# Kernel optimization log

Measured on AMD Instinct MI355X. Metric: run time of the kernel, lower is better.

## Reference

```python
import jax, jax.numpy as jnp
import numpy as np

NPOINT = 2048
RADII = (0.4, 0.8)
NSAMPLES = (16, 32)
EPS = 1e-5


def _fps(xyz, npoint):
    # iterative farthest point sampling, start at index 0 (matches CUDA kernel)
    B, N, _ = xyz.shape

    def step(carry, _):
        dist, last = carry  # dist [B,N], last [B]
        lx = jnp.take_along_axis(xyz, last[:, None, None], axis=1)  # [B,1,3]
        d = jnp.sum((xyz - lx) ** 2, axis=-1)  # [B,N]
        dist = jnp.minimum(dist, d)
        nxt = jnp.argmax(dist, axis=1).astype(jnp.int32)
        return (dist, nxt), last

    init = (jnp.full((B, N), 1e10, xyz.dtype), jnp.zeros((B,), jnp.int32))
    _, idxs = jax.lax.scan(step, init, None, length=npoint)
    return idxs.T  # [B, npoint]


def _ball_query(radius, nsample, xyz, new_xyz):
    # first-nsample points within radius, in original order; pad with first hit (0 if none)
    N = xyz.shape[1]
    d2 = jnp.sum((new_xyz[:, :, None, :] - xyz[:, None, :, :]) ** 2, axis=-1)  # [B,S,N]
    mask = d2 < radius * radius
    ar = jnp.arange(N, dtype=jnp.int32)
    key = jnp.where(mask, ar, N + ar)  # in-range first, stable original order
    order = jnp.argsort(key, axis=-1)[..., :nsample].astype(jnp.int32)  # [B,S,ns]
    cnt = mask.sum(axis=-1, keepdims=True)  # [B,S,1]
    valid = jnp.arange(nsample) < cnt
    return jnp.where(valid, order, order[..., :1])


def _bn_relu(x):
    # training-mode BatchNorm (gamma=1, beta=0) over all dims but channel (last)
    red = tuple(range(x.ndim - 1))
    mu = x.mean(axis=red, keepdims=True)
    var = x.var(axis=red, keepdims=True)
    return jax.nn.relu((x - mu) * jax.lax.rsqrt(var + EPS))


def _scale(xyz, new_xyz, feats, radius, nsample, ws):
    idx = _ball_query(radius, nsample, xyz, new_xyz)  # [B,S,ns]
    B, S, ns = idx.shape
    flat = idx.reshape(B, S * ns)
    gx = jnp.take_along_axis(xyz, flat[..., None], axis=1).reshape(B, S, ns, 3)
    gx = gx - new_xyz[:, :, None, :]  # relative coords
    gf = jnp.take_along_axis(feats, flat[..., None], axis=1).reshape(B, S, ns, -1)
    h = jnp.concatenate([gx, gf], axis=-1)  # [B,S,ns,3+C]
    for w in ws:
        h = _bn_relu(h @ w)  # pointwise conv (kernel 1) + BN + ReLU
    return h.max(axis=2)  # max-pool over group -> [B,S,Cout]


def setup_inputs() -> dict:
    key = jax.random.key(0)
    ks = jax.random.split(key, 16)
    s = 0.02
    return {
        "xyz": jax.random.normal(ks[0], (8, 8192, 3), jnp.float32),
        "features": jax.random.normal(ks[1], (8, 8192, 64), jnp.float32),
        "w0_0": jax.random.normal(ks[2], (67, 64), jnp.float32) * s,
        "w0_1": jax.random.normal(ks[3], (64, 64), jnp.float32) * s,
        "w0_2": jax.random.normal(ks[4], (64, 128), jnp.float32) * s,
        "w1_0": jax.random.normal(ks[5], (67, 64), jnp.float32) * s,
        "w1_1": jax.random.normal(ks[6], (64, 64), jnp.float32) * s,
        "w1_2": jax.random.normal(ks[7], (64, 128), jnp.float32) * s,
        "agg_w": jax.random.normal(ks[8], (256, 256), jnp.float32) * s,
        "agg_b": jax.random.normal(ks[9], (256,), jnp.float32) * s,
        "conf_w": jax.random.normal(ks[10], (256, 256), jnp.float32) * s,
        "cls_w": jax.random.normal(ks[11], (256, 3), jnp.float32) * s,
        "cls_b": jax.random.normal(ks[12], (3,), jnp.float32) * s,
    }


def reference(xyz, features, w0_0, w0_1, w0_2, w1_0, w1_1, w1_2,
              agg_w, agg_b, conf_w, cls_w, cls_b):
    idx = _fps(xyz, NPOINT)  # [B,S]
    new_xyz = jnp.take_along_axis(xyz, idx[..., None], axis=1)  # [B,S,3]
    f0 = _scale(xyz, new_xyz, features, RADII[0], NSAMPLES[0], (w0_0, w0_1, w0_2))
    f1 = _scale(xyz, new_xyz, features, RADII[1], NSAMPLES[1], (w1_0, w1_1, w1_2))
    h = jnp.concatenate([f0, f1], axis=-1)  # [B,S,256]
    h = _bn_relu(h @ agg_w + agg_b)  # aggregation Linear + BN + ReLU
    c = _bn_relu(h @ conf_w)  # confidence hidden layer
    cls = c @ cls_w + cls_b  # [B,S,num_class]
    return new_xyz, h, cls
```

## Files before the change

### kernel.cpp

```cpp
#include <hip/hip_runtime.h>
#include <cstdint>
#include <cstddef>

constexpr int Bb = 8;
constexpr int Nn = 8192;
constexpr int Ss = 2048;
constexpr int BS = Bb * Ss;

typedef float vfloat2 __attribute__((ext_vector_type(2)));

__global__ __launch_bounds__(1024) void fps_kernel(const float* __restrict__ xyz,
                                                   float* __restrict__ new_xyz) {
  __shared__ float lx[Nn * 3];
  __shared__ int sidx[Ss];
  __shared__ unsigned long long slotV[2];
  __shared__ int slotI[2];
  const int b = blockIdx.x;
  const int tid = threadIdx.x;
  const float* xb = xyz + (size_t)b * Nn * 3;
  for (int e = tid; e < Nn * 3; e += 1024) lx[e] = xb[e];
  if (tid == 0) {
    slotV[0] = 0ull; slotV[1] = 0ull;
    slotI[0] = 0x7fffffff; slotI[1] = 0x7fffffff;
  }
  __syncthreads();

  vfloat2 px2[4], py2[4], pz2[4], df2[4];
  double dist[8];
#pragma unroll
  for (int jj = 0; jj < 4; ++jj) {
    const int p0 = tid + (2 * jj) * 1024, p1 = tid + (2 * jj + 1) * 1024;
    px2[jj] = (vfloat2){lx[p0 * 3 + 0], lx[p1 * 3 + 0]};
    py2[jj] = (vfloat2){lx[p0 * 3 + 1], lx[p1 * 3 + 1]};
    pz2[jj] = (vfloat2){lx[p0 * 3 + 2], lx[p1 * 3 + 2]};
    df2[jj] = (vfloat2){3.0e38f, 3.0e38f};
    dist[2 * jj] = 1e10;
    dist[2 * jj + 1] = 1e10;
  }
  float lmax = 3.0e38f;
  int cur = 0;
  double lv = -1.0;
  int li = 0x7fffffff;
  float lv32 = -1.0f;
  float wv32_c = -1.0f;
  for (int i = 0; i < Ss; ++i) {
    if (tid == 0) sidx[i] = cur;
    const float cxf = lx[cur * 3 + 0], cyf = lx[cur * 3 + 1], czf = lx[cur * 3 + 2];
    const vfloat2 cx2 = {cxf, cxf}, cy2 = {cyf, cyf}, cz2 = {czf, czf};
    vfloat2 d2v[4];
#pragma unroll
    for (int jj = 0; jj < 4; ++jj) {
      const vfloat2 dx = px2[jj] - cx2;
      const vfloat2 dy = py2[jj] - cy2;
      const vfloat2 dz = pz2[jj] - cz2;
      d2v[jj] = dx * dx + dy * dy + dz * dz;
    }
    const float dmin = fminf(fminf(fminf(d2v[0].x, d2v[0].y), fminf(d2v[1].x, d2v[1].y)),
                             fminf(fminf(d2v[2].x, d2v[2].y), fminf(d2v[3].x, d2v[3].y)));
    bool changed = false;
    if (dmin <= lmax) {
#pragma unroll
      for (int j = 0; j < 8; ++j) {
        const float d2s = d2v[j >> 1][j & 1];
        const float dfs = (j & 1) ? df2[j >> 1].y : df2[j >> 1].x;
        if (d2s <= dfs) {
          const float pxs = px2[j >> 1][j & 1];
          const float pys = py2[j >> 1][j & 1];
          const float pzs = pz2[j >> 1][j & 1];
          double dx = __dsub_rn((double)pxs, (double)cxf);
          double dy = __dsub_rn((double)pys, (double)cyf);
          double dz = __dsub_rn((double)pzs, (double)czf);
          double d = __dadd_rn(__dadd_rn(__dmul_rn(dx, dx), __dmul_rn(dy, dy)),
                               __dmul_rn(dz, dz));
          if (d < dist[j]) {
            dist[j] = d;
            const float dfn = (float)d * 1.000002f;
            if (j & 1) df2[j >> 1].y = dfn; else df2[j >> 1].x = dfn;
            changed = true;
          }
        }
      }
      if (changed) {
        lv = -1.0;
        li = 0;
#pragma unroll
        for (int j = 0; j < 8; ++j) {
          if (dist[j] > lv) { lv = dist[j]; li = tid + j * 1024; }
        }
        lv32 = (float)lv;
        lmax = fmaxf(fmaxf(fmaxf(df2[0].x, df2[0].y), fmaxf(df2[1].x, df2[1].y)),
                     fmaxf(fmaxf(df2[2].x, df2[2].y), fmaxf(df2[3].x, df2[3].y)));
      }
    }
    const unsigned long long anyb = __ballot(changed);
    if (anyb) {
      float m32 = lv32;
#pragma unroll
      for (int off = 1; off < 64; off <<= 1) m32 = fmaxf(m32, __shfl_xor(m32, off));
      wv32_c = m32;
    }
    const int pb = i & 1;
    if (lv32 == wv32_c) atomicMax(&slotV[pb], (unsigned long long)__double_as_longlong(lv));
    __syncthreads();
    const double W = __longlong_as_double((long long)slotV[pb]);
    if (lv == W) atomicMin(&slotI[pb], li);
    if (tid == 0) {
      slotV[pb ^ 1] = 0ull;
      slotI[pb ^ 1] = 0x7fffffff;
    }
    __syncthreads();
    cur = slotI[pb];
  }
  __syncthreads();
  float* nxb = new_xyz + (size_t)b * Ss * 3;
  for (int e = tid; e < Ss * 3; e += 1024) {
    const int i = e / 3, c = e - i * 3;
    nxb[e] = lx[sidx[i] * 3 + c];
  }
}

__global__ __launch_bounds__(256) void ballq_kernel(const float* __restrict__ xyz,
                                                    const float* __restrict__ nxyz,
                                                    int* __restrict__ idx0,
                                                    int* __restrict__ idx1) {
  const int wid = threadIdx.x >> 6, lane = threadIdx.x & 63;
  const int bs = blockIdx.x * 4 + wid;
  const int b = bs >> 11;
  const float* xb = xyz + (size_t)b * Nn * 3;
  const double cx = (double)nxyz[bs * 3 + 0];
  const double cy = (double)nxyz[bs * 3 + 1];
  const double cz = (double)nxyz[bs * 3 + 2];
  const double R0 = 0.4 * 0.4, R1 = 0.8 * 0.8;
  int cnt0 = 0, cnt1 = 0, first0 = 0, first1 = 0;
  const unsigned long long lmask = (1ull << lane) - 1ull;
  for (int base = 0; base < Nn; base += 64) {
    const int p = base + lane;
    double dx = __dsub_rn((double)xb[p * 3 + 0], cx);
    double dy = __dsub_rn((double)xb[p * 3 + 1], cy);
    double dz = __dsub_rn((double)xb[p * 3 + 2], cz);
    double d2 = __dadd_rn(__dadd_rn(__dmul_rn(dx, dx), __dmul_rn(dy, dy)), __dmul_rn(dz, dz));
    const bool in0 = d2 < R0, in1 = d2 < R1;
    unsigned long long m0 = __ballot(in0);
    unsigned long long m1 = __ballot(in1);
    if (cnt0 < 16 && m0) {
      if (cnt0 == 0) first0 = base + __builtin_ctzll(m0);
      int r = (int)__popcll(m0 & lmask);
      if (in0 && cnt0 + r < 16) idx0[bs * 16 + cnt0 + r] = p;
      cnt0 += (int)__popcll(m0);
    }
    if (cnt1 < 32 && m1) {
      if (cnt1 == 0) first1 = base + __builtin_ctzll(m1);
      int r = (int)__popcll(m1 & lmask);
      if (in1 && cnt1 + r < 32) idx1[bs * 32 + cnt1 + r] = p;
      cnt1 += (int)__popcll(m1);
    }
    if (cnt0 >= 16 && cnt1 >= 32) break;
  }
  const int f0 = cnt0 < 16 ? cnt0 : 16;
  for (int j = f0 + lane; j < 16; j += 64) idx0[bs * 16 + j] = first0;
  const int f1 = cnt1 < 32 ? cnt1 : 32;
  for (int j = f1 + lane; j < 32; j += 64) idx1[bs * 32 + j] = first1;
}

template <int COUT, int KTOT, int MODE, int NS, bool POOL, bool BIAS>
__global__ __launch_bounds__(256) void mlp_gemm(
    const float* __restrict__ xin, const float* __restrict__ xin2,
    const float* __restrict__ bnp, const float* __restrict__ bnp2,
    const float* __restrict__ w, const float* __restrict__ bias,
    const int* __restrict__ gidx, const float* __restrict__ xyz,
    const float* __restrict__ nxyz, const float* __restrict__ feats,
    float* __restrict__ hw, float* __restrict__ out, float* __restrict__ P) {
  constexpr int KC = (KTOT <= 68) ? KTOT : 32;
  constexpr int NCH = (KTOT + KC - 1) / KC;
  constexpr int TC = COUT / 16;
  constexpr int XPAD = KC + 1;
  constexpr int XSZ = 64 * XPAD;
  constexpr int EPI = (POOL ? 48 : 32) * COUT;
  constexpr int SM = (XSZ + KC * COUT > EPI) ? (XSZ + KC * COUT) : EPI;
  __shared__ float smem[SM];
  float* xS = smem;
  float* wS = smem + XSZ;

  const int tid = threadIdx.x;
  const int cg = tid & 15, rg = tid >> 4;
  const int row0 = blockIdx.x * 64;
  float acc[4][TC];
#pragma unroll
  for (int i = 0; i < 4; ++i)
#pragma unroll
    for (int t = 0; t < TC; ++t) acc[i][t] = 0.f;

  for (int ch = 0; ch < NCH; ++ch) {
    const int k0 = ch * KC;
    if (ch) __syncthreads();
    for (int e = tid; e < 64 * KC; e += 256) {
      const int r = e / KC, kk = e - r * KC;
      const int kg = k0 + kk;
      const int rowg = row0 + r;
      float v;
      if constexpr (MODE == 0) {
        const int bs = rowg / NS;
        const int p = gidx[rowg];
        const int bb = bs >> 11;
        if (kg < 3)
          v = xyz[(bb * Nn + p) * 3 + kg] - nxyz[bs * 3 + kg];
        else
          v = feats[((bb * Nn + p) << 6) + (kg - 3)];
      } else if constexpr (MODE == 1) {
        v = fmaxf((xin[(size_t)rowg * 64 + kg] - bnp[kg]) * bnp[64 + kg], 0.f);
      } else if constexpr (MODE == 2) {
        if (kg < 128)
          v = fmaxf((xin[(size_t)rowg * 128 + kg] - bnp[kg]) * bnp[128 + kg], 0.f);
        else {
          const int k2 = kg - 128;
          v = fmaxf((xin2[(size_t)rowg * 128 + k2] - bnp2[k2]) * bnp2[128 + k2], 0.f);
        }
      } else {
        v = fmaxf((xin[(size_t)rowg * 256 + kg] - bnp[kg]) * bnp[256 + kg], 0.f);
        hw[(size_t)rowg * 256 + kg] = v;
      }
      xS[r * XPAD + kk] = v;
    }
    for (int e = tid; e < KC * COUT; e += 256) {
      const int kk = e / COUT, c = e - kk * COUT;
      wS[kk * COUT + c] = w[(size_t)(k0 + kk) * COUT + c];
    }
    __syncthreads();
    for (int kk = 0; kk < KC; ++kk) {
      float xr[4];
#pragma unroll
      for (int i = 0; i < 4; ++i) xr[i] = xS[(rg * 4 + i) * XPAD + kk];
#pragma unroll
      for (int t = 0; t < TC; t += 4) {
        const float4 wv = *(const float4*)&wS[kk * COUT + cg * TC + t];
#pragma unroll
        for (int i = 0; i < 4; ++i) {
          acc[i][t + 0] = fmaf(xr[i], wv.x, acc[i][t + 0]);
          acc[i][t + 1] = fmaf(xr[i], wv.y, acc[i][t + 1]);
          acc[i][t + 2] = fmaf(xr[i], wv.z, acc[i][t + 2]);
          acc[i][t + 3] = fmaf(xr[i], wv.w, acc[i][t + 3]);
        }
      }
    }
  }
  __syncthreads();
  if constexpr (BIAS) {
#pragma unroll
    for (int t = 0; t < TC; ++t) {
      const float bv = bias[cg * TC + t];
#pragma unroll
      for (int i = 0; i < 4; ++i) acc[i][t] += bv;
    }
  }
  float* ssum = smem;
  float* ssq = smem + 16 * COUT;
  float* pbuf = smem + 32 * COUT;
  const int colb = cg * TC;
#pragma unroll
  for (int t = 0; t < TC; ++t) {
    float s = 0.f, q = 0.f, m = -3.4e38f;
#pragma unroll
    for (int i = 0; i < 4; ++i) {
      const float v = acc[i][t];
      s += v;
      q = fmaf(v, v, q);
      m = fmaxf(m, v);
    }
    ssum[rg * COUT + colb + t] = s;
    ssq[rg * COUT + colb + t] = q;
    if constexpr (POOL) pbuf[rg * COUT + colb + t] = m;
  }
  __syncthreads();
  const int gX = gridDim.x;
  for (int c = tid; c < COUT; c += 256) {
    float s = 0.f, q = 0.f;
#pragma unroll
    for (int rr = 0; rr < 16; ++rr) {
      s += ssum[rr * COUT + c];
      q += ssq[rr * COUT + c];
    }
    P[(size_t)c * gX + blockIdx.x] = s;
    P[(size_t)(COUT + c) * gX + blockIdx.x] = q;
  }
  if constexpr (POOL) {
    constexpr int G = 64 / NS, RPG = NS / 4;
    for (int o = tid; o < G * COUT; o += 256) {
      const int g = o / COUT, c = o - g * COUT;
      float m = pbuf[(g * RPG) * COUT + c];
#pragma unroll
      for (int qq = 1; qq < RPG; ++qq) m = fmaxf(m, pbuf[(g * RPG + qq) * COUT + c]);
      out[(size_t)(blockIdx.x * G + g) * COUT + c] = m;
    }
  } else {
#pragma unroll
    for (int i = 0; i < 4; ++i) {
      float* op = out + (size_t)(row0 + rg * 4 + i) * COUT + colb;
#pragma unroll
      for (int t = 0; t < TC; t += 4) {
        *(float4*)(op + t) = make_float4(acc[i][t], acc[i][t + 1], acc[i][t + 2], acc[i][t + 3]);
      }
    }
  }
}

__global__ __launch_bounds__(256) void bn_finalize(const float* __restrict__ P, int gX,
                                                   int M, int C, float* __restrict__ bnp) {
  __shared__ double sh[512];
  const int c = blockIdx.x;
  const int tid = threadIdx.x;
  const float* psum = P + (size_t)c * gX;
  const float* psq = P + (size_t)(C + c) * gX;
  double s = 0, q = 0;
  for (int i = tid; i < gX; i += 256) {
    s += (double)psum[i];
    q += (double)psq[i];
  }
  sh[tid] = s;
  sh[256 + tid] = q;
  __syncthreads();
  for (int off = 128; off; off >>= 1) {
    if (tid < off) {
      sh[tid] += sh[tid + off];
      sh[256 + tid] += sh[256 + tid + off];
    }
    __syncthreads();
  }
  if (tid == 0) {
    const double invM = 1.0 / (double)M;
    const double mu = sh[0] * invM;
    const double var = sh[256] * invM - mu * mu;
    bnp[c] = (float)mu;
    bnp[C + c] = (float)(1.0 / sqrt(var + 1e-5));
  }
}

__global__ __launch_bounds__(256) void cls_kernel(const float* __restrict__ craw,
                                                  const float* __restrict__ bnp,
                                                  const float* __restrict__ clsw,
                                                  const float* __restrict__ clsb,
                                                  float* __restrict__ outc) {
  const int wid = threadIdx.x >> 6, lane = threadIdx.x & 63;
  const int row = blockIdx.x * 4 + wid;
  const float* cr = craw + (size_t)row * 256;
  float a0 = 0.f, a1 = 0.f, a2 = 0.f;
#pragma unroll 4
  for (int k = lane; k < 256; k += 64) {
    float x = fmaxf((cr[k] - bnp[k]) * bnp[256 + k], 0.f);
    a0 = fmaf(x, clsw[k * 3 + 0], a0);
    a1 = fmaf(x, clsw[k * 3 + 1], a1);
    a2 = fmaf(x, clsw[k * 3 + 2], a2);
  }
#pragma unroll
  for (int off = 32; off; off >>= 1) {
    a0 += __shfl_down(a0, off);
    a1 += __shfl_down(a1, off);
    a2 += __shfl_down(a2, off);
  }
  if (lane == 0) {
    outc[row * 3 + 0] = a0 + clsb[0];
    outc[row * 3 + 1] = a1 + clsb[1];
    outc[row * 3 + 2] = a2 + clsb[2];
  }
}

extern "C" void kernel_launch(void* const* d_in, const int* in_sizes, int n_in,
                              void* d_out, int out_size, void* d_ws, size_t ws_size,
                              hipStream_t stream) {
  (void)in_sizes; (void)n_in; (void)out_size; (void)ws_size;
  const float* xyz = (const float*)d_in[0];
  const float* feats = (const float*)d_in[1];
  const float* w00 = (const float*)d_in[2];
  const float* w01 = (const float*)d_in[3];
  const float* w02 = (const float*)d_in[4];
  const float* w10 = (const float*)d_in[5];
  const float* w11 = (const float*)d_in[6];
  const float* w12 = (const float*)d_in[7];
  const float* aggw = (const float*)d_in[8];
  const float* aggb = (const float*)d_in[9];
  const float* confw = (const float*)d_in[10];
  const float* clsw = (const float*)d_in[11];
  const float* clsb = (const float*)d_in[12];

  float* outp = (float*)d_out;
  float* nxyz = outp;
  float* hout = outp + (size_t)BS * 3;
  float* clsout = hout + (size_t)BS * 256;

  char* ws = (char*)d_ws;
  const size_t MB = 1u << 20;
  int* idx0 = (int*)(ws + 0);
  int* idx1 = (int*)(ws + 1 * MB);
  float* bnb = (float*)(ws + 3 * MB);
  float* P = (float*)(ws + 4 * MB);
  float* pool0 = (float*)(ws + 12 * MB);
  float* pool1 = (float*)(ws + 20 * MB);
  float* aggraw = (float*)(ws + 28 * MB);
  float* confraw = (float*)(ws + 44 * MB);
  float* hA = (float*)(ws + 60 * MB);

  fps_kernel<<<Bb, 1024, 0, stream>>>(xyz, nxyz);
  ballq_kernel<<<BS / 4, 256, 0, stream>>>(xyz, nxyz, idx0, idx1);

  mlp_gemm<64, 67, 0, 16, false, false><<<4096, 256, 0, stream>>>(
      nullptr, nullptr, nullptr, nullptr, w00, nullptr, idx0, xyz, nxyz, feats, nullptr, hA, P);
  bn_finalize<<<64, 256, 0, stream>>>(P, 4096, 262144, 64, bnb + 0);
  mlp_gemm<64, 64, 1, 1, false, false><<<4096, 256, 0, stream>>>(
      hA, nullptr, bnb + 0, nullptr, w01, nullptr, nullptr, nullptr, nullptr, nullptr, nullptr, hA, P);
  bn_finalize<<<64, 256, 0, stream>>>(P, 4096, 262144, 64, bnb + 128);
  mlp_gemm<128, 64, 1, 16, true, false><<<4096, 256, 0, stream>>>(
      hA, nullptr, bnb + 128, nullptr, w02, nullptr, nullptr, nullptr, nullptr, nullptr, nullptr, pool0, P);
  bn_finalize<<<128, 256, 0, stream>>>(P, 4096, 262144, 128, bnb + 256);

  mlp_gemm<64, 67, 0, 32, false, false><<<8192, 256, 0, stream>>>(
      nullptr, nullptr, nullptr, nullptr, w10, nullptr, idx1, xyz, nxyz, feats, nullptr, hA, P);
  bn_finalize<<<64, 256, 0, stream>>>(P, 8192, 524288, 64, bnb + 512);
  mlp_gemm<64, 64, 1, 1, false, false><<<8192, 256, 0, stream>>>(
      hA, nullptr, bnb + 512, nullptr, w11, nullptr, nullptr, nullptr, nullptr, nullptr, nullptr, hA, P);
  bn_finalize<<<64, 256, 0, stream>>>(P, 8192, 524288, 64, bnb + 640);
  mlp_gemm<128, 64, 1, 32, true, false><<<8192, 256, 0, stream>>>(
      hA, nullptr, bnb + 640, nullptr, w12, nullptr, nullptr, nullptr, nullptr, nullptr, nullptr, pool1, P);
  bn_finalize<<<128, 256, 0, stream>>>(P, 8192, 524288, 128, bnb + 768);

  mlp_gemm<256, 256, 2, 1, false, true><<<256, 256, 0, stream>>>(
      pool0, pool1, bnb + 256, bnb + 768, aggw, aggb, nullptr, nullptr, nullptr, nullptr, nullptr, aggraw, P);
  bn_finalize<<<256, 256, 0, stream>>>(P, 256, 16384, 256, bnb + 1024);

  mlp_gemm<256, 256, 4, 1, false, false><<<256, 256, 0, stream>>>(
      aggraw, nullptr, bnb + 1024, nullptr, confw, nullptr, nullptr, nullptr, nullptr, nullptr, hout, confraw, P);
  bn_finalize<<<256, 256, 0, stream>>>(P, 256, 16384, 256, bnb + 1536);

  cls_kernel<<<BS / 4, 256, 0, stream>>>(confraw, bnb + 1536, clsw, clsb, clsout);
}
```

Baseline: 3.762 ms.

## Replace BN finalize kernels with atomic stats and in-kernel normalization; narrow FPS reduction trigger

Removes the separate bn_finalize launches. Each GEMM block now atomically adds its per-channel sum and sum-of-squares into a zeroed stats buffer, and the consuming kernel computes mean and rsqrt into shared memory in its prologue. This cuts eight small launches and their partial-sum round trips. The cost is contention on float atomics, variance now computed in float instead of double (precision risk), and nondeterministic summation order. The FPS loop also does the wave max-shuffle only when a lane holding the previous wave maximum changed, skipping most shuffle reductions.

```diff
diff --git a/kernel.cpp b/kernel.cpp
--- a/kernel.cpp
+++ b/kernel.cpp
@@ -47,6 +47,7 @@
     if (tid == 0) sidx[i] = cur;
     const float cxf = lx[cur * 3 + 0], cyf = lx[cur * 3 + 1], czf = lx[cur * 3 + 2];
     const vfloat2 cx2 = {cxf, cxf}, cy2 = {cyf, cyf}, cz2 = {czf, czf};
+    const bool wasTop = (lv32 == wv32_c);
     vfloat2 d2v[4];
 #pragma unroll
     for (int jj = 0; jj < 4; ++jj) {
@@ -92,8 +93,8 @@
                      fmaxf(fmaxf(df2[2].x, df2[2].y), fmaxf(df2[3].x, df2[3].y)));
       }
     }
-    const unsigned long long anyb = __ballot(changed);
-    if (anyb) {
+    const unsigned long long topChanged = __ballot(changed && wasTop);
+    if (topChanged) {
       float m32 = lv32;
 #pragma unroll
       for (int off = 1; off < 64; off <<= 1) m32 = fmaxf(m32, __shfl_xor(m32, off));
@@ -165,11 +166,12 @@
 template <int COUT, int KTOT, int MODE, int NS, bool POOL, bool BIAS>
 __global__ __launch_bounds__(256) void mlp_gemm(
     const float* __restrict__ xin, const float* __restrict__ xin2,
-    const float* __restrict__ bnp, const float* __restrict__ bnp2,
+    const float* __restrict__ stIn, const float* __restrict__ stIn2,
+    float invM1, float invM2,
     const float* __restrict__ w, const float* __restrict__ bias,
     const int* __restrict__ gidx, const float* __restrict__ xyz,
     const float* __restrict__ nxyz, const float* __restrict__ feats,
-    float* __restrict__ hw, float* __restrict__ out, float* __restrict__ P) {
+    float* __restrict__ hw, float* __restrict__ out, float* __restrict__ Sout) {
   constexpr int KC = (KTOT <= 68) ? KTOT : 32;
   constexpr int NCH = (KTOT + KC - 1) / KC;
   constexpr int TC = COUT / 16;
@@ -177,13 +179,35 @@
   constexpr int XSZ = 64 * XPAD;
   constexpr int EPI = (POOL ? 48 : 32) * COUT;
   constexpr int SM = (XSZ + KC * COUT > EPI) ? (XSZ + KC * COUT) : EPI;
-  __shared__ float smem[SM];
+  constexpr int BNSZ = (MODE == 0) ? 0 : 512;
+  __shared__ float smem[SM + BNSZ];
   float* xS = smem;
   float* wS = smem + XSZ;
+  float* bnM = smem + SM;
+  float* bnR = smem + SM + 256;
 
   const int tid = threadIdx.x;
   const int cg = tid & 15, rg = tid >> 4;
   const int row0 = blockIdx.x * 64;
+
+  if constexpr (MODE != 0) {
+    for (int c = tid; c < KTOT; c += 256) {
+      float sum, sq, im;
+      if constexpr (MODE == 2) {
+        if (c < 128) { sum = stIn[c]; sq = stIn[128 + c]; im = invM1; }
+        else { sum = stIn2[c - 128]; sq = stIn2[c]; im = invM2; }
+      } else {
+        constexpr int C = (MODE == 1) ? 64 : 256;
+        sum = stIn[c]; sq = stIn[C + c]; im = invM1;
+      }
+      const float mu = sum * im;
+      const float var = sq * im - mu * mu;
+      bnM[c] = mu;
+      bnR[c] = 1.0f / sqrtf(var + 1e-5f);
+    }
+    __syncthreads();
+  }
+
   float acc[4][TC];
 #pragma unroll
   for (int i = 0; i < 4; ++i)
@@ -207,16 +231,14 @@
         else
           v = feats[((bb * Nn + p) << 6) + (kg - 3)];
       } else if constexpr (MODE == 1) {
-        v = fmaxf((xin[(size_t)rowg * 64 + kg] - bnp[kg]) * bnp[64 + kg], 0.f);
+        v = fmaxf((xin[(size_t)rowg * 64 + kg] - bnM[kg]) * bnR[kg], 0.f);
       } else if constexpr (MODE == 2) {
         if (kg < 128)
-          v = fmaxf((xin[(size_t)rowg * 128 + kg] - bnp[kg]) * bnp[128 + kg], 0.f);
-        else {
-          const int k2 = kg - 128;
-          v = fmaxf((xin2[(size_t)rowg * 128 + k2] - bnp2[k2]) * bnp2[128 + k2], 0.f);
-        }
+          v = fmaxf((xin[(size_t)rowg * 128 + kg] - bnM[kg]) * bnR[kg], 0.f);
+        else
+          v = fmaxf((xin2[(size_t)rowg * 128 + (kg - 128)] - bnM[kg]) * bnR[kg], 0.f);
       } else {
-        v = fmaxf((xin[(size_t)rowg * 256 + kg] - bnp[kg]) * bnp[256 + kg], 0.f);
+        v = fmaxf((xin[(size_t)rowg * 256 + kg] - bnM[kg]) * bnR[kg], 0.f);
         hw[(size_t)rowg * 256 + kg] = v;
       }
       xS[r * XPAD + kk] = v;
@@ -271,7 +293,6 @@
     if constexpr (POOL) pbuf[rg * COUT + colb + t] = m;
   }
   __syncthreads();
-  const int gX = gridDim.x;
   for (int c = tid; c < COUT; c += 256) {
     float s = 0.f, q = 0.f;
 #pragma unroll
@@ -279,8 +300,8 @@
       s += ssum[rr * COUT + c];
       q += ssq[rr * COUT + c];
     }
-    P[(size_t)c * gX + blockIdx.x] = s;
-    P[(size_t)(COUT + c) * gX + blockIdx.x] = q;
+    atomicAdd(&Sout[c], s);
+    atomicAdd(&Sout[COUT + c], q);
   }
   if constexpr (POOL) {
     constexpr int G = 64 / NS, RPG = NS / 4;
@@ -303,49 +324,29 @@
   }
 }
 
-__global__ __launch_bounds__(256) void bn_finalize(const float* __restrict__ P, int gX,
-                                                   int M, int C, float* __restrict__ bnp) {
-  __shared__ double sh[512];
-  const int c = blockIdx.x;
-  const int tid = threadIdx.x;
-  const float* psum = P + (size_t)c * gX;
-  const float* psq = P + (size_t)(C + c) * gX;
-  double s = 0, q = 0;
-  for (int i = tid; i < gX; i += 256) {
-    s += (double)psum[i];
-    q += (double)psq[i];
-  }
-  sh[tid] = s;
-  sh[256 + tid] = q;
-  __syncthreads();
-  for (int off = 128; off; off >>= 1) {
-    if (tid < off) {
-      sh[tid] += sh[tid + off];
-      sh[256 + tid] += sh[256 + tid + off];
-    }
-    __syncthreads();
-  }
-  if (tid == 0) {
-    const double invM = 1.0 / (double)M;
-    const double mu = sh[0] * invM;
-    const double var = sh[256] * invM - mu * mu;
-    bnp[c] = (float)mu;
-    bnp[C + c] = (float)(1.0 / sqrt(var + 1e-5));
-  }
-}
-
 __global__ __launch_bounds__(256) void cls_kernel(const float* __restrict__ craw,
-                                                  const float* __restrict__ bnp,
+                                                  const float* __restrict__ st,
                                                   const float* __restrict__ clsw,
                                                   const float* __restrict__ clsb,
                                                   float* __restrict__ outc) {
-  const int wid = threadIdx.x >> 6, lane = threadIdx.x & 63;
+  __shared__ float bnM[256], bnR[256];
+  const int tid = threadIdx.x;
+  {
+    const float im = 1.0f / 16384.0f;
+    const float sum = st[tid], sq = st[256 + tid];
+    const float mu = sum * im;
+    const float var = sq * im - mu * mu;
+    bnM[tid] = mu;
+    bnR[tid] = 1.0f / sqrtf(var + 1e-5f);
+  }
+  __syncthreads();
+  const int wid = tid >> 6, lane = tid & 63;
   const int row = blockIdx.x * 4 + wid;
   const float* cr = craw + (size_t)row * 256;
   float a0 = 0.f, a1 = 0.f, a2 = 0.f;
 #pragma unroll 4
   for (int k = lane; k < 256; k += 64) {
-    float x = fmaxf((cr[k] - bnp[k]) * bnp[256 + k], 0.f);
+    float x = fmaxf((cr[k] - bnM[k]) * bnR[k], 0.f);
     a0 = fmaf(x, clsw[k * 3 + 0], a0);
     a1 = fmaf(x, clsw[k * 3 + 1], a1);
     a2 = fmaf(x, clsw[k * 3 + 2], a2);
@@ -390,44 +391,49 @@
   const size_t MB = 1u << 20;
   int* idx0 = (int*)(ws + 0);
   int* idx1 = (int*)(ws + 1 * MB);
-  float* bnb = (float*)(ws + 3 * MB);
-  float* P = (float*)(ws + 4 * MB);
+  float* st = (float*)(ws + 3 * MB);
   float* pool0 = (float*)(ws + 12 * MB);
   float* pool1 = (float*)(ws + 20 * MB);
   float* aggraw = (float*)(ws + 28 * MB);
   float* confraw = (float*)(ws + 44 * MB);
   float* hA = (float*)(ws + 60 * MB);
 
+  hipMemsetAsync(st, 0, 2048 * sizeof(float), stream);
+
+  const float iM0 = 1.0f / 262144.0f;
+  const float iM1 = 1.0f / 524288.0f;
+  const float iMh = 1.0f / 16384.0f;
+
   fps_kernel<<<Bb, 1024, 0, stream>>>(xyz, nxyz);
   ballq_kernel<<<BS / 4, 256, 0, stream>>>(xyz, nxyz, idx0, idx1);
 
   mlp_gemm<64, 67, 0, 16, false, false><<<4096, 256, 0, stream>>>(
-      nullptr, nullptr, nullptr, nullptr, w00, nullptr, idx0, xyz, nxyz, feats, nullptr, hA, P);
-  bn_finalize<<<64, 256, 0, stream>>>(P, 4096, 262144, 64, bnb + 0);
+      nullptr, nullptr, nullptr, nullptr, 0.f, 0.f, w00, nullptr,
+      idx0, xyz, nxyz, feats, nullptr, hA, st + 0);
   mlp_gemm<64, 64, 1, 1, false, false><<<4096, 256, 0, stream>>>(
-      hA, nullptr, bnb + 0, nullptr, w01, nullptr, nullptr, nullptr, nullptr, nullptr, nullptr, hA, P);
-  bn_finalize<<<64, 256, 0, stream>>>(P, 4096, 262144, 64, bnb + 128);
+      hA, nullptr, st + 0, nullptr, iM0, 0.f, w01, nullptr,
+      nullptr, nullptr, nullptr, nullptr, nullptr, hA, st + 128);
   mlp_gemm<128, 64, 1, 16, true, false><<<4096, 256, 0, stream>>>(
-      hA, nullptr, bnb + 128, nullptr, w02, nullptr, nullptr, nullptr, nullptr, nullptr, nullptr, pool0, P);
-  bn_finalize<<<128, 256, 0, stream>>>(P, 4096, 262144, 128, bnb + 256);
+      hA, nullptr, st + 128, nullptr, iM0, 0.f, w02, nullptr,
+      nullptr, nullptr, nullptr, nullptr, nullptr, pool0, st + 256);
 
   mlp_gemm<64, 67, 0, 32, false, false><<<8192, 256, 0, stream>>>(
-      nullptr, nullptr, nullptr, nullptr, w10, nullptr, idx1, xyz, nxyz, feats, nullptr, hA, P);
-  bn_finalize<<<64, 256, 0, stream>>>(P, 8192, 524288, 64, bnb + 512);
+      nullptr, nullptr, nullptr, nullptr, 0.f, 0.f, w10, nullptr,
+      idx1, xyz, nxyz, feats, nullptr, hA, st + 512);
   mlp_gemm<64, 64, 1, 1, false, false><<<8192, 256, 0, stream>>>(
-      hA, nullptr, bnb + 512, nullptr, w11, nullptr, nullptr, nullptr, nullptr, nullptr, nullptr, hA, P);
-  bn_finalize<<<64, 256, 0, stream>>>(P, 8192, 524288, 64, bnb + 640);
+      hA, nullptr, st + 512, nullptr, iM1, 0.f, w11, nullptr,
+      nullptr, nullptr, nullptr, nullptr, nullptr, hA, st + 640);
   mlp_gemm<128, 64, 1, 32, true, false><<<8192, 256, 0, stream>>>(
-      hA, nullptr, bnb + 640, nullptr, w12, nullptr, nullptr, nullptr, nullptr, nullptr, nullptr, pool1, P);
-  bn_finalize<<<128, 256, 0, stream>>>(P, 8192, 524288, 128, bnb + 768);
+      hA, nullptr, st + 640, nullptr, iM1, 0.f, w12, nullptr,
+      nullptr, nullptr, nullptr, nullptr, nullptr, pool1, st + 768);
 
   mlp_gemm<256, 256, 2, 1, false, true><<<256, 256, 0, stream>>>(
-      pool0, pool1, bnb + 256, bnb + 768, aggw, aggb, nullptr, nullptr, nullptr, nullptr, nullptr, aggraw, P);
-  bn_finalize<<<256, 256, 0, stream>>>(P, 256, 16384, 256, bnb + 1024);
+      pool0, pool1, st + 256, st + 768, iM0, iM1, aggw, aggb,
+      nullptr, nullptr, nullptr, nullptr, nullptr, aggraw, st + 1024);
 
   mlp_gemm<256, 256, 4, 1, false, false><<<256, 256, 0, stream>>>(
-      aggraw, nullptr, bnb + 1024, nullptr, confw, nullptr, nullptr, nullptr, nullptr, nullptr, hout, confraw, P);
-  bn_finalize<<<256, 256, 0, stream>>>(P, 256, 16384, 256, bnb + 1536);
-
-  cls_kernel<<<BS / 4, 256, 0, stream>>>(confraw, bnb + 1536, clsw, clsb, clsout);
+      aggraw, nullptr, st + 1024, nullptr, iMh, 0.f, confw, nullptr,
+      nullptr, nullptr, nullptr, nullptr, hout, confraw, st + 1536);
+
+  cls_kernel<<<BS / 4, 256, 0, stream>>>(confraw, st + 1536, clsw, clsb, clsout);
 }
```

After: 3.959 ms. 5.2% more time.
